# Optimization experiments

Measured on AMD Instinct MI355X. Metric: run time of the kernel, lower is better.

Reference implementation:

```python
import jax, jax.numpy as jnp
import numpy as np

B = 1024
INPUT_DIM = 768
NUM_CLASSES = 5
NUM_PRIMARY_CAPS = 32
PRIMARY_CAP_DIM = 8
ROUTING_CAP_DIM = 16
NUM_ITER = 3
PROJ_DIM = 256 * 6 * 6  # 9216
NUM_IN_CAPS = NUM_PRIMARY_CAPS * 16  # conv output is 4x4 spatial -> 512


def squash(t, axis=-1):
    sq = jnp.sum(t * t, axis=axis, keepdims=True)
    scale = sq / (1.0 + sq)
    return scale * t / jnp.sqrt(sq + 1e-8)


def setup_inputs() -> dict:
    key = jax.random.key(0)
    k = jax.random.split(key, 6)
    x = jax.random.normal(k[0], (B, INPUT_DIM), dtype=jnp.float32)
    W1 = jax.random.normal(k[1], (INPUT_DIM, PROJ_DIM), dtype=jnp.float32) * 0.02
    b1 = jnp.zeros((PROJ_DIM,), dtype=jnp.float32)
    convW = jax.random.normal(k[2], (NUM_PRIMARY_CAPS * PRIMARY_CAP_DIM, 256, 3, 3), dtype=jnp.float32) * 0.02  # OIHW
    convB = jnp.zeros((NUM_PRIMARY_CAPS * PRIMARY_CAP_DIM,), dtype=jnp.float32)
    # matches torch.randn init in RoutingCapsules: [num_in, num_out, out_dim, in_dim]
    Wr = jax.random.normal(k[3], (NUM_IN_CAPS, NUM_CLASSES, ROUTING_CAP_DIM, PRIMARY_CAP_DIM), dtype=jnp.float32)
    return {"x": x, "W1": W1, "b1": b1, "convW": convW, "convB": convB, "Wr": Wr}


def reference(x, W1, b1, convW, convB, Wr):
    # feature projection (dropout is identity in eval)
    h = jax.nn.relu(x @ W1 + b1)
    h = h.reshape(-1, 256, 6, 6)
    # primary capsules conv: k=3, s=1, pad=0 -> [B, 256, 4, 4]
    out = jax.lax.conv_general_dilated(h, convW, window_strides=(1, 1), padding='VALID',
                                       dimension_numbers=('NCHW', 'OIHW', 'NCHW'))
    out = out + convB[None, :, None, None]
    bsz = out.shape[0]
    out = out.reshape(bsz, NUM_PRIMARY_CAPS, PRIMARY_CAP_DIM, -1)      # [B,32,8,16]
    out = jnp.transpose(out, (0, 1, 3, 2)).reshape(bsz, -1, PRIMARY_CAP_DIM)  # [B,512,8]
    u = squash(out, axis=-1)
    # prediction vectors u_hat: [B, in_caps, out_caps, out_dim]
    u_hat = jnp.einsum('nodi,bni->bnod', Wr, u)
    # dynamic routing
    b_logits = jnp.zeros((bsz, NUM_IN_CAPS, NUM_CLASSES, 1), dtype=u_hat.dtype)
    v = None
    for it in range(NUM_ITER):
        c = jax.nn.softmax(b_logits, axis=2)
        s = jnp.sum(c * u_hat, axis=1)  # [B, out_caps, out_dim]
        v = squash(s, axis=-1)
        if it < NUM_ITER - 1:
            agreement = jnp.sum(u_hat * v[:, None], axis=-1, keepdims=True)
            b_logits = b_logits + agreement
    class_probs = jnp.sqrt(jnp.sum(v * v, axis=-1))
    return (class_probs, v)
```

## Files before the change

### kernel.cpp

```cpp
#include <hip/hip_runtime.h>
#include <hip/hip_fp16.h>

#define BSZ   1024
#define INDIM 768
#define PROJ  9216
#define NCAP  512
#define NCLS  5
#define K2    2304

typedef __bf16    bf16x8 __attribute__((ext_vector_type(8)));
typedef _Float16  f16x8  __attribute__((ext_vector_type(8)));
typedef float     f32x4  __attribute__((ext_vector_type(4)));
typedef _Float16  h2     __attribute__((ext_vector_type(2)));

static __device__ __forceinline__ unsigned short f2bf(float f) {
  unsigned int x = __float_as_uint(f);
  return (unsigned short)((x + 0x7fffu + ((x >> 16) & 1u)) >> 16);
}
static __device__ __forceinline__ unsigned short f2h(float f) {
  return __builtin_bit_cast(unsigned short, (_Float16)f);
}

#if defined(__has_builtin)
#if __has_builtin(__builtin_amdgcn_fdot2)
#define HAVE_FDOT2 1
#endif
#endif
static __device__ __forceinline__ float fdot2(h2 a, h2 b, float c) {
#ifdef HAVE_FDOT2
  return __builtin_amdgcn_fdot2(a, b, c, false);
#else
  return c + (float)a[0] * (float)b[0] + (float)a[1] * (float)b[1];
#endif
}
static __device__ __forceinline__ h2 u2h2(unsigned int u) {
  return __builtin_bit_cast(h2, u);
}

static __device__ __forceinline__ void gload16(const void* g, void* l) {
  auto gp = reinterpret_cast<const unsigned int __attribute__((address_space(1)))*>(
      (unsigned long long)g);
  auto lp = reinterpret_cast<unsigned int __attribute__((address_space(3)))*>(
      (unsigned long long)l);
  __builtin_amdgcn_global_load_lds(gp, lp, 16, 0, 0);
}

__global__ __launch_bounds__(256) void mfma_gemm_bk64(
    const unsigned short* __restrict__ A,
    const unsigned short* __restrict__ Bt,
    const float* __restrict__ bias,
    unsigned short* __restrict__ Cout,
    int M, int N, int K) {
  __shared__ __align__(16) unsigned short smem[32768];
  const int t    = threadIdx.x;
  const int bn   = blockIdx.x * 128;
  const int bm   = blockIdx.y * 128;
  const int lane = t & 63, wid = t >> 6;
  const int wm   = (wid >> 1) * 64;
  const int wn   = (wid & 1) * 64;
  const int l15  = lane & 15, kb = lane >> 4;

  const unsigned short* asrc[4];
  const unsigned short* bsrc[4];
#pragma unroll
  for (int cc = 0; cc < 4; ++cc) {
    const int c = t + cc * 256;
    const int row = c >> 3, seg = c & 7;
    const int sk = (seg ^ (row & 7)) << 3;
    asrc[cc] = A  + (size_t)(bm + row) * K + sk;
    bsrc[cc] = Bt + (size_t)(bn + row) * K + sk;
  }

  int aoff[4][2], boff[4][2];
#pragma unroll
  for (int i = 0; i < 4; ++i)
#pragma unroll
    for (int kk = 0; kk < 2; ++kk) {
      const int ra = wm + i * 16 + l15, sa = kk * 4 + kb;
      aoff[i][kk] = ra * 64 + ((sa ^ (ra & 7)) << 3);
      const int rb = wn + i * 16 + l15;
      boff[i][kk] = 8192 + rb * 64 + ((sa ^ (rb & 7)) << 3);
    }

  f32x4 acc[4][4];
#pragma unroll
  for (int i = 0; i < 4; ++i)
#pragma unroll
    for (int j = 0; j < 4; ++j)
#pragma unroll
      for (int q = 0; q < 4; ++q) acc[i][j][q] = 0.f;

  const int nk = K >> 6;
  auto stage = [&](int ks, int buf) {
    const int ko = ks << 6;
    unsigned short* sb = &smem[buf * 16384];
#pragma unroll
    for (int cc = 0; cc < 4; ++cc) {
      gload16(asrc[cc] + ko, sb + (t + cc * 256) * 8);
      gload16(bsrc[cc] + ko, sb + 8192 + (t + cc * 256) * 8);
    }
  };

  stage(0, 0);
  __syncthreads();

  int buf = 0;
  for (int ks = 0; ks < nk; ++ks) {
    if (ks + 1 < nk) stage(ks + 1, buf ^ 1);
    const unsigned short* base = &smem[buf * 16384];
    bf16x8 af[4][2], bfr[4][2];
#pragma unroll
    for (int i = 0; i < 4; ++i)
#pragma unroll
      for (int kk = 0; kk < 2; ++kk) {
        af[i][kk]  = *(const bf16x8*)(base + aoff[i][kk]);
        bfr[i][kk] = *(const bf16x8*)(base + boff[i][kk]);
      }
#pragma unroll
    for (int kk = 0; kk < 2; ++kk)
#pragma unroll
      for (int i = 0; i < 4; ++i)
#pragma unroll
        for (int j = 0; j < 4; ++j)
          acc[i][j] = __builtin_amdgcn_mfma_f32_16x16x32_bf16(af[i][kk], bfr[j][kk], acc[i][j], 0, 0, 0);
    __syncthreads();
    buf ^= 1;
  }

#pragma unroll
  for (int j = 0; j < 4; ++j) {
    const int col = bn + wn + j * 16 + l15;
    const float bv = bias[col];
#pragma unroll
    for (int i = 0; i < 4; ++i)
#pragma unroll
      for (int q = 0; q < 4; ++q) {
        const int row = bm + wm + i * 16 + kb * 4 + q;
        Cout[(size_t)row * N + col] = f2bf(fmaxf(acc[i][j][q] + bv, 0.f));
      }
  }
}

__global__ __launch_bounds__(256) void conv_gemm_sq(
    const unsigned short* __restrict__ ht,
    const unsigned short* __restrict__ Wt2,
    const float* __restrict__ convB,
    unsigned short* __restrict__ U) {
  __shared__ __align__(16) unsigned short smem[24576];
  const int t    = threadIdx.x;
  const int bn   = blockIdx.x * 128;
  const int bm   = blockIdx.y * 64;
  const int lane = t & 63, wid = t >> 6;
  const int l15  = lane & 15, kb = lane >> 4;

  const unsigned short* asrc[2];
#pragma unroll
  for (int cc = 0; cc < 2; ++cc) {
    const int c = t + cc * 256;
    const int row = c >> 3, seg = c & 7;
    const int gr = bm + row, b = gr >> 4, p = gr & 15;
    const int spb = (p >> 2) * 6 + (p & 3);
    asrc[cc] = ht + (size_t)b * PROJ + spb * 256 + ((seg ^ (row & 7)) << 3);
  }
  const unsigned short* bsrc[4];
#pragma unroll
  for (int cc = 0; cc < 4; ++cc) {
    const int c = t + cc * 256;
    const int row = c >> 3, seg = c & 7;
    bsrc[cc] = Wt2 + (size_t)(bn + row) * K2 + ((seg ^ (row & 7)) << 3);
  }

  int aoff[4][2], boff[2][2];
#pragma unroll
  for (int i = 0; i < 4; ++i)
#pragma unroll
    for (int kk = 0; kk < 2; ++kk) {
      const int row = i * 16 + l15, seg = kk * 4 + kb;
      aoff[i][kk] = row * 64 + ((seg ^ (row & 7)) << 3);
    }
#pragma unroll
  for (int j = 0; j < 2; ++j)
#pragma unroll
    for (int kk = 0; kk < 2; ++kk) {
      const int row = wid * 32 + j * 16 + l15, seg = kk * 4 + kb;
      boff[j][kk] = 4096 + row * 64 + ((seg ^ (row & 7)) << 3);
    }

  f32x4 acc[4][2];
#pragma unroll
  for (int i = 0; i < 4; ++i)
#pragma unroll
    for (int j = 0; j < 2; ++j)
#pragma unroll
      for (int q = 0; q < 4; ++q) acc[i][j][q] = 0.f;

  auto stage = [&](int ks, int buf) {
    const int tap  = ks >> 2;
    const int aofs = (tap + 3 * (tap / 3)) * 256 + ((ks & 3) << 6);
    const int bofs = ks << 6;
    unsigned short* sb = &smem[buf * 12288];
    gload16(asrc[0] + aofs, sb + t * 8);
    gload16(asrc[1] + aofs, sb + t * 8 + 2048);
    gload16(bsrc[0] + bofs, sb + 4096 + t * 8);
    gload16(bsrc[1] + bofs, sb + 4096 + t * 8 + 2048);
    gload16(bsrc[2] + bofs, sb + 4096 + t * 8 + 4096);
    gload16(bsrc[3] + bofs, sb + 4096 + t * 8 + 6144);
  };

  stage(0, 0);
  __syncthreads();

  int buf = 0;
  for (int ks = 0; ks < 36; ++ks) {
    if (ks + 1 < 36) stage(ks + 1, buf ^ 1);
    const unsigned short* base = &smem[buf * 12288];
    bf16x8 af[4][2], bfr[2][2];
#pragma unroll
    for (int i = 0; i < 4; ++i)
#pragma unroll
      for (int kk = 0; kk < 2; ++kk) af[i][kk] = *(const bf16x8*)(base + aoff[i][kk]);
#pragma unroll
    for (int j = 0; j < 2; ++j)
#pragma unroll
      for (int kk = 0; kk < 2; ++kk) bfr[j][kk] = *(const bf16x8*)(base + boff[j][kk]);
#pragma unroll
    for (int kk = 0; kk < 2; ++kk)
#pragma unroll
      for (int i = 0; i < 4; ++i)
#pragma unroll
        for (int j = 0; j < 2; ++j)
          acc[i][j] = __builtin_amdgcn_mfma_f32_16x16x32_bf16(af[i][kk], bfr[j][kk], acc[i][j], 0, 0, 0);
    __syncthreads();
    buf ^= 1;
  }

#pragma unroll
  for (int j = 0; j < 2; ++j) {
    const int oc  = bn + wid * 32 + j * 16 + l15;
    const int cap = oc >> 3, ii = oc & 7;
    const float bv = convB[oc];
#pragma unroll
    for (int i = 0; i < 4; ++i) {
#pragma unroll
      for (int q = 0; q < 4; ++q) {
        const int row = bm + i * 16 + kb * 4 + q;
        const int b = row >> 4, p = row & 15;
        const float val = acc[i][j][q] + bv;
        float sq = val * val;
        sq += __shfl_xor(sq, 1);
        sq += __shfl_xor(sq, 2);
        sq += __shfl_xor(sq, 4);
        const float scale = sq / (1.f + sq) / sqrtf(sq + 1e-8f);
        U[(size_t)b * 4096 + cap * 128 + p * 8 + ii] = f2h(val * scale);
      }
    }
  }
}

#define TP_BLOCKS (288 * 24)
#define NX_ITEMS (BSZ * INDIM / 4)
#define NW_ITEMS (NCAP * 640 / 4)
#define NWT_ITEMS (NCAP * 80)
#define NC_ITEMS 65536
#define NB_ITEMS PROJ
#define EW_TOTAL (NX_ITEMS + NW_ITEMS + NWT_ITEMS + NC_ITEMS + NB_ITEMS)
#define EW_BLOCKS (EW_TOTAL / 256)

__global__ __launch_bounds__(256) void prep_all(
    const float* __restrict__ W1, unsigned short* __restrict__ w1t,
    const float* __restrict__ x, unsigned short* __restrict__ xb,
    const float* __restrict__ Wr, __half2* __restrict__ wrh,
    unsigned short* __restrict__ wrh_t,
    const float* __restrict__ convW, unsigned short* __restrict__ wt2,
    const float* __restrict__ b1, float* __restrict__ pb1) {
  __shared__ float tile[32][33];
  if (blockIdx.x < TP_BLOCKS) {
    const int tb = blockIdx.x;
    const int n0 = (tb % 288) * 32, k0 = (tb / 288) * 32;
    const int r = threadIdx.x >> 3, c = (threadIdx.x & 7) * 4;
    float4 v = *(const float4*)(W1 + (size_t)(k0 + r) * PROJ + n0 + c);
    tile[r][c] = v.x; tile[r][c + 1] = v.y; tile[r][c + 2] = v.z; tile[r][c + 3] = v.w;
    __syncthreads();
    ushort4 o;
    o.x = f2bf(tile[c + 0][r]); o.y = f2bf(tile[c + 1][r]);
    o.z = f2bf(tile[c + 2][r]); o.w = f2bf(tile[c + 3][r]);
    const int nn = n0 + r;
    const int prow = (nn % 36) * 256 + nn / 36;
    *(ushort4*)(w1t + (size_t)prow * INDIM + k0 + c) = o;
    return;
  }
  const int id = (blockIdx.x - TP_BLOCKS) * 256 + threadIdx.x;
  if (id < NX_ITEMS) {
    float4 v = ((const float4*)x)[id];
    ushort4 o;
    o.x = f2bf(v.x); o.y = f2bf(v.y); o.z = f2bf(v.z); o.w = f2bf(v.w);
    ((ushort4*)xb)[id] = o;
  } else if (id < NX_ITEMS + NW_ITEMS) {
    const int i = id - NX_ITEMS;
    float4 v = ((const float4*)Wr)[i];
    wrh[i * 2]     = __floats2half2_rn(v.x, v.y);
    wrh[i * 2 + 1] = __floats2half2_rn(v.z, v.w);
  } else if (id < NX_ITEMS + NW_ITEMS + NWT_ITEMS) {
    const int i = id - NX_ITEMS - NW_ITEMS;
    const int od = i / NCAP, n = i % NCAP;
    const float4 a = *(const float4*)(Wr + (size_t)n * 640 + od * 8);
    const float4 b = *(const float4*)(Wr + (size_t)n * 640 + od * 8 + 4);
    __half2 h0 = __floats2half2_rn(a.x, a.y), h1 = __floats2half2_rn(a.z, a.w);
    __half2 h2v = __floats2half2_rn(b.x, b.y), h3 = __floats2half2_rn(b.z, b.w);
    uint4 st = make_uint4(__builtin_bit_cast(unsigned int, h0),
                          __builtin_bit_cast(unsigned int, h1),
                          __builtin_bit_cast(unsigned int, h2v),
                          __builtin_bit_cast(unsigned int, h3));
    *(uint4*)(wrh_t + (size_t)od * 4096 + n * 8) = st;
  } else if (id < NX_ITEMS + NW_ITEMS + NWT_ITEMS + NC_ITEMS) {
    const int i = id - NX_ITEMS - NW_ITEMS - NWT_ITEMS;
    const int oc = i >> 8, ic = i & 255;
    const float* s = convW + (size_t)i * 9;
#pragma unroll
    for (int tap = 0; tap < 9; ++tap)
      wt2[(size_t)oc * K2 + tap * 256 + ic] = f2bf(s[tap]);
  } else if (id < EW_TOTAL) {
    const int n = id - NX_ITEMS - NW_ITEMS - NWT_ITEMS - NC_ITEMS;
    pb1[(n % 36) * 256 + n / 36] = b1[n];
  }
}

__global__ __launch_bounds__(256) void s0v0_gemm(
    const unsigned short* __restrict__ U,
    const unsigned short* __restrict__ WrhT,
    float* __restrict__ v0) {
  __shared__ float red[4][16][16];
  __shared__ float sl[16][17];
  __shared__ float scl[16];
  const int bt = blockIdx.x, o = blockIdx.y;
  const int t = threadIdx.x, wid = t >> 6, lane = t & 63;
  const int l15 = lane & 15, kb = lane >> 4;
  const int gb = bt * 16;

  f32x4 acc;
  acc[0] = 0.f; acc[1] = 0.f; acc[2] = 0.f; acc[3] = 0.f;
  const unsigned short* abase = WrhT + (size_t)(o * 16 + l15) * 4096 + kb * 8;
  const unsigned short* bbase = U + (size_t)(gb + l15) * 4096 + kb * 8;
  const int k0b = wid * 1024;
#pragma unroll 4
  for (int k0 = k0b; k0 < k0b + 1024; k0 += 32) {
    const f16x8 av = __builtin_bit_cast(f16x8, *(const uint4*)(abase + k0));
    const f16x8 bv = __builtin_bit_cast(f16x8, *(const uint4*)(bbase + k0));
    acc = __builtin_amdgcn_mfma_f32_16x16x32_f16(av, bv, acc, 0, 0, 0);
  }
#pragma unroll
  for (int q = 0; q < 4; ++q) red[wid][kb * 4 + q][l15] = acc[q];
  __syncthreads();
  const int row = t >> 4, col = t & 15;
  const float s = 0.2f * (red[0][row][col] + red[1][row][col] +
                          red[2][row][col] + red[3][row][col]);
  sl[row][col] = s;
  __syncthreads();
  if (t < 16) {
    float sq = 0.f;
#pragma unroll
    for (int r = 0; r < 16; ++r) { const float xx = sl[r][t]; sq += xx * xx; }
    scl[t] = sq / (1.f + sq) / sqrtf(sq + 1e-8f);
  }
  __syncthreads();
  v0[(size_t)(gb + col) * 80 + o * 16 + row] = s * scl[col];
}

__global__ __launch_bounds__(512) void uhat_p1(
    const unsigned short* __restrict__ U,
    const unsigned short* __restrict__ Wrh,
    const float* __restrict__ v0,
    unsigned short* __restrict__ uhat,
    float* __restrict__ sp1,
    int b0, int CB) {
  __shared__ float sred[8][16][80];
  const int mt = blockIdx.x, q = blockIdx.y;
  const int t = threadIdx.x, wid = t >> 6, lane = t & 63;
  const int l15 = lane & 15, kb = lane >> 4;
  const int bm = mt * 16;
  const int gb = b0 + bm;

  f32x4 vreg[5];
#pragma unroll
  for (int jn = 0; jn < 5; ++jn)
    vreg[jn] = *(const f32x4*)(v0 + (size_t)(gb + l15) * 80 + jn * 16 + kb * 4);

  f32x4 sacc[5];
#pragma unroll
  for (int jn = 0; jn < 5; ++jn)
#pragma unroll
    for (int qq = 0; qq < 4; ++qq) sacc[jn][qq] = 0.f;

  const uint4 zz = make_uint4(0, 0, 0, 0);
#pragma unroll
  for (int i = 0; i < 8; ++i) {
    const int n = q * 64 + wid * 8 + i;
    uint4 av = zz;
    if (kb == 0) av = *(const uint4*)(U + (size_t)(gb + l15) * 4096 + n * 8);
    const f16x8 uf = __builtin_bit_cast(f16x8, av);
    f32x4 cfr[5];
#pragma unroll
    for (int jn = 0; jn < 5; ++jn) {
      uint4 wv = zz;
      if (kb == 0) wv = *(const uint4*)(Wrh + (size_t)n * 640 + (jn * 16 + l15) * 8);
      f32x4 z;
      z[0] = 0.f; z[1] = 0.f; z[2] = 0.f; z[3] = 0.f;
      cfr[jn] = __builtin_amdgcn_mfma_f32_16x16x32_f16(
          __builtin_bit_cast(f16x8, wv), uf, z, 0, 0, 0);
      ushort4 st;
      st.x = f2h(cfr[jn][0]); st.y = f2h(cfr[jn][1]);
      st.z = f2h(cfr[jn][2]); st.w = f2h(cfr[jn][3]);
      *(ushort4*)(uhat + ((size_t)(bm + l15) * 512 + n) * 80 + jn * 16 + kb * 4) = st;
    }
    float a[5];
#pragma unroll
    for (int jn = 0; jn < 5; ++jn) {
      float d = cfr[jn][0] * vreg[jn][0] + cfr[jn][1] * vreg[jn][1] +
                cfr[jn][2] * vreg[jn][2] + cfr[jn][3] * vreg[jn][3];
      d += __shfl_xor(d, 16);
      d += __shfl_xor(d, 32);
      a[jn] = d;
    }
    float m = fmaxf(fmaxf(fmaxf(a[0], a[1]), fmaxf(a[2], a[3])), a[4]);
    float c[5], es = 0.f;
#pragma unroll
    for (int o = 0; o < 5; ++o) { c[o] = __expf(a[o] - m); es += c[o]; }
    const float inv = 1.f / es;
#pragma unroll
    for (int jn = 0; jn < 5; ++jn) {
      const float cc = c[jn] * inv;
#pragma unroll
      for (int qq = 0; qq < 4; ++qq) sacc[jn][qq] += cc * cfr[jn][qq];
    }
  }

#pragma unroll
  for (int jn = 0; jn < 5; ++jn)
#pragma unroll
    for (int qq = 0; qq < 4; ++qq)
      sred[wid][l15][jn * 16 + kb * 4 + qq] = sacc[jn][qq];
  __syncthreads();
#pragma unroll
  for (int k = 0; k < 3; ++k) {
    const int id = t + k * 512;
    if (id < 1280) {
      const int bb = id / 80, od = id % 80;
      float val = 0.f;
#pragma unroll
      for (int w = 0; w < 8; ++w) val += sred[w][bb][od];
      sp1[((size_t)q * BSZ + gb + bb) * 80 + od] = val;
    }
  }
}

__global__ __launch_bounds__(128) void v01_k(
    const float* __restrict__ sp1, const float* __restrict__ v0,
    float* __restrict__ v01, int b0) {
  const int b = b0 + blockIdx.x, t = threadIdx.x;
  if (t < 80) {
    float s = 0.f;
#pragma unroll
    for (int g = 0; g < 8; ++g) s += sp1[((size_t)g * BSZ + b) * 80 + t];
    float sq = s * s;
    sq += __shfl_xor(sq, 1);
    sq += __shfl_xor(sq, 2);
    sq += __shfl_xor(sq, 4);
    sq += __shfl_xor(sq, 8);
    const float scale = sq / (1.f + sq) / sqrtf(sq + 1e-8f);
    v01[(size_t)b * 80 + t] = v0[(size_t)b * 80 + t] + s * scale;
  }
}

__global__ __launch_bounds__(256) void route_pass2(
    const unsigned short* __restrict__ uhat,
    const float* __restrict__ vsum_in,
    float* __restrict__ out, int b0) {
  __shared__ unsigned int vph2[40];
  __shared__ float red[4][2][40];
  const int bl = blockIdx.x;
  const int b  = b0 + bl;
  const int t  = threadIdx.x;

  float v0r = 0.f;
  if (t < 80) {
    v0r = vsum_in[(size_t)b * 80 + t];
    const float vnext = __shfl_down(v0r, 1);
    if ((t & 1) == 0)
      vph2[t >> 1] = __builtin_bit_cast(unsigned int, __floats2half2_rn(v0r, vnext));
  }
  __syncthreads();

  const int p = t >> 1, h = t & 1;
  float acc[5][8];
#pragma unroll
  for (int o = 0; o < 5; ++o)
#pragma unroll
    for (int j = 0; j < 8; ++j) acc[o][j] = 0.f;

  const unsigned short* ub = uhat + (size_t)bl * 40960;
  for (int c4 = 0; c4 < 4; ++c4) {
    const int n = c4 * 128 + p;
    const unsigned short* row = ub + n * 80 + h * 8;
    uint4 uv[5];
#pragma unroll
    for (int o = 0; o < 5; ++o) uv[o] = *(const uint4*)(row + o * 16);
    float ap[5];
#pragma unroll
    for (int o = 0; o < 5; ++o) {
      const int vb = o * 8 + h * 4;
      float a = fdot2(u2h2(uv[o].x), u2h2(vph2[vb]), 0.f);
      a = fdot2(u2h2(uv[o].y), u2h2(vph2[vb + 1]), a);
      a = fdot2(u2h2(uv[o].z), u2h2(vph2[vb + 2]), a);
      a = fdot2(u2h2(uv[o].w), u2h2(vph2[vb + 3]), a);
      ap[o] = a + __shfl_xor(a, 1);
    }
    float m = ap[0];
#pragma unroll
    for (int o = 1; o < 5; ++o) m = fmaxf(m, ap[o]);
    float es = 0.f, e[5];
#pragma unroll
    for (int o = 0; o < 5; ++o) { e[o] = __expf(ap[o] - m); es += e[o]; }
    const float inv = 1.f / es;
#pragma unroll
    for (int o = 0; o < 5; ++o) {
      const float cc = e[o] * inv;
      h2 hx = u2h2(uv[o].x), hy = u2h2(uv[o].y), hz = u2h2(uv[o].z), hw = u2h2(uv[o].w);
      acc[o][0] += cc * (float)hx[0]; acc[o][1] += cc * (float)hx[1];
      acc[o][2] += cc * (float)hy[0]; acc[o][3] += cc * (float)hy[1];
      acc[o][4] += cc * (float)hz[0]; acc[o][5] += cc * (float)hz[1];
      acc[o][6] += cc * (float)hw[0]; acc[o][7] += cc * (float)hw[1];
    }
  }

#pragma unroll
  for (int off = 2; off <= 32; off <<= 1)
#pragma unroll
    for (int o = 0; o < 5; ++o)
#pragma unroll
      for (int j = 0; j < 8; ++j) acc[o][j] += __shfl_xor(acc[o][j], off);
  const int wid = t >> 6, lane = t & 63;
  if (lane < 2) {
#pragma unroll
    for (int o = 0; o < 5; ++o)
#pragma unroll
      for (int j = 0; j < 8; ++j) red[wid][lane][o * 8 + j] = acc[o][j];
  }
  __syncthreads();

  if (t < 80) {
    const int o = t >> 4, d = t & 15, hh = d >> 3, dl = d & 7;
    const int c = o * 8 + dl;
    float s = red[0][hh][c] + red[1][hh][c] + red[2][hh][c] + red[3][hh][c];
    float sq = s * s;
    sq += __shfl_xor(sq, 1);
    sq += __shfl_xor(sq, 2);
    sq += __shfl_xor(sq, 4);
    sq += __shfl_xor(sq, 8);
    const float scale = sq / (1.f + sq) / sqrtf(sq + 1e-8f);
    const float vn = s * scale;
    out[5 * BSZ + (size_t)b * 80 + t] = vn;
    float vv = vn * vn;
    vv += __shfl_xor(vv, 1);
    vv += __shfl_xor(vv, 2);
    vv += __shfl_xor(vv, 4);
    vv += __shfl_xor(vv, 8);
    if ((t & 15) == 0) out[(size_t)b * 5 + o] = sqrtf(vv);
  }
}

extern "C" void kernel_launch(void* const* d_in, const int* in_sizes, int n_in,
                              void* d_out, int out_size, void* d_ws, size_t ws_size,
                              hipStream_t stream) {
  const float* x     = (const float*)d_in[0];
  const float* W1    = (const float*)d_in[1];
  const float* b1    = (const float*)d_in[2];
  const float* convW = (const float*)d_in[3];
  const float* convB = (const float*)d_in[4];
  const float* Wr    = (const float*)d_in[5];
  float* out = (float*)d_out;

  char* base = (char*)d_ws;
  size_t off = 0;
  auto alloc = [&](size_t bytes) { size_t o = off; off = (off + bytes + 255) & ~(size_t)255; return o; };
  const size_t o_wrh  = alloc((size_t)NCAP * 640 * 2);
  const size_t o_wrt  = alloc((size_t)80 * 4096 * 2);
  const size_t o_u    = alloc((size_t)BSZ * 4096 * 2);
  const size_t o_sp1  = alloc((size_t)8 * BSZ * 80 * 4);
  const size_t o_v0   = alloc((size_t)BSZ * 80 * 4);
  const size_t o_v01  = alloc((size_t)BSZ * 80 * 4);
  const size_t o_pool = off;
  size_t poff = o_pool;
  auto palloc = [&](size_t bytes) { size_t o = poff; poff = (poff + bytes + 255) & ~(size_t)255; return o; };
  const size_t o_ht  = palloc((size_t)BSZ * PROJ * 2);
  const size_t o_w1t = palloc((size_t)PROJ * INDIM * 2);
  const size_t o_xb  = palloc((size_t)BSZ * INDIM * 2);
  const size_t o_wt2 = palloc((size_t)256 * K2 * 2);
  const size_t o_pb1 = palloc((size_t)PROJ * 4);

  unsigned short* ht   = (unsigned short*)(base + o_ht);
  unsigned short* w1t  = (unsigned short*)(base + o_w1t);
  unsigned short* xb   = (unsigned short*)(base + o_xb);
  unsigned short* wt2  = (unsigned short*)(base + o_wt2);
  float*          pb1  = (float*)(base + o_pb1);
  unsigned short* wrh  = (unsigned short*)(base + o_wrh);
  unsigned short* wrt  = (unsigned short*)(base + o_wrt);
  unsigned short* u    = (unsigned short*)(base + o_u);
  float*          sp1  = (float*)(base + o_sp1);
  float*          v0   = (float*)(base + o_v0);
  float*          v01  = (float*)(base + o_v01);
  unsigned short* uhat = (unsigned short*)(base + o_pool);

  prep_all<<<TP_BLOCKS + EW_BLOCKS, 256, 0, stream>>>(
      W1, w1t, x, xb, Wr, (__half2*)wrh, wrt, convW, wt2, b1, pb1);

  mfma_gemm_bk64<<<dim3(PROJ / 128, BSZ / 128), 256, 0, stream>>>(
      xb, w1t, pb1, ht, BSZ, PROJ, INDIM);

  conv_gemm_sq<<<dim3(2, 256), 256, 0, stream>>>(ht, wt2, convB, u);

  s0v0_gemm<<<dim3(BSZ / 16, 5), 256, 0, stream>>>(u, wrt, v0);

  const size_t pool_sz = ws_size > o_pool ? ws_size - o_pool : 0;
  int CB = 1024;
  while (CB > 16 && (size_t)CB * 512 * 80 * 2 > pool_sz) CB >>= 1;
  for (int b0 = 0; b0 < BSZ; b0 += CB) {
    uhat_p1<<<dim3(CB / 16, 8), 512, 0, stream>>>(u, wrh, v0, uhat, sp1, b0, CB);
    v01_k<<<CB, 128, 0, stream>>>(sp1, v0, v01, b0);
    route_pass2<<<CB, 256, 0, stream>>>(uhat, v01, out, b0);
  }
}
```

Measured before the change: 152.4 us.

## Shrink conv GEMM tile to 64x64 and regroup uhat layout per 16-sample tile

The primary-capsule conv GEMM tile shrinks from 64x128 to 64x64 with a 2x2 warp grid, doubling the block count from 512 to 1024 and cutting shared memory per block. This is meant to improve occupancy and load balance across CUs, at the cost of less operand reuse per block. Separately, the uhat buffer is re-laid out as [tile][capsule][16 samples][80] so the MFMA store in uhat_p1 writes contiguous rows. route_pass2 indexing is updated to match, giving it a 1280-element stride between capsules.

```diff
diff --git a/kernel.cpp b/kernel.cpp
--- a/kernel.cpp
+++ b/kernel.cpp
@@ -141,19 +141,21 @@
   }
 }
 
-__global__ __launch_bounds__(256) void conv_gemm_sq(
+__global__ __launch_bounds__(256) void conv_gemm_sq64(
     const unsigned short* __restrict__ ht,
     const unsigned short* __restrict__ Wt2,
     const float* __restrict__ convB,
     unsigned short* __restrict__ U) {
-  __shared__ __align__(16) unsigned short smem[24576];
+  __shared__ __align__(16) unsigned short smem[16384];
   const int t    = threadIdx.x;
-  const int bn   = blockIdx.x * 128;
+  const int bn   = blockIdx.x * 64;
   const int bm   = blockIdx.y * 64;
   const int lane = t & 63, wid = t >> 6;
+  const int wm   = (wid >> 1) * 32, wn = (wid & 1) * 32;
   const int l15  = lane & 15, kb = lane >> 4;
 
   const unsigned short* asrc[2];
+  const unsigned short* bsrc[2];
 #pragma unroll
   for (int cc = 0; cc < 2; ++cc) {
     const int c = t + cc * 256;
@@ -161,34 +163,23 @@
     const int gr = bm + row, b = gr >> 4, p = gr & 15;
     const int spb = (p >> 2) * 6 + (p & 3);
     asrc[cc] = ht + (size_t)b * PROJ + spb * 256 + ((seg ^ (row & 7)) << 3);
-  }
-  const unsigned short* bsrc[4];
-#pragma unroll
-  for (int cc = 0; cc < 4; ++cc) {
-    const int c = t + cc * 256;
-    const int row = c >> 3, seg = c & 7;
     bsrc[cc] = Wt2 + (size_t)(bn + row) * K2 + ((seg ^ (row & 7)) << 3);
   }
 
-  int aoff[4][2], boff[2][2];
-#pragma unroll
-  for (int i = 0; i < 4; ++i)
+  int aoff[2][2], boff[2][2];
+#pragma unroll
+  for (int i = 0; i < 2; ++i)
 #pragma unroll
     for (int kk = 0; kk < 2; ++kk) {
-      const int row = i * 16 + l15, seg = kk * 4 + kb;
-      aoff[i][kk] = row * 64 + ((seg ^ (row & 7)) << 3);
-    }
-#pragma unroll
-  for (int j = 0; j < 2; ++j)
-#pragma unroll
-    for (int kk = 0; kk < 2; ++kk) {
-      const int row = wid * 32 + j * 16 + l15, seg = kk * 4 + kb;
-      boff[j][kk] = 4096 + row * 64 + ((seg ^ (row & 7)) << 3);
-    }
-
-  f32x4 acc[4][2];
-#pragma unroll
-  for (int i = 0; i < 4; ++i)
+      const int ra = wm + i * 16 + l15, sa = kk * 4 + kb;
+      aoff[i][kk] = ra * 64 + ((sa ^ (ra & 7)) << 3);
+      const int rb = wn + i * 16 + l15;
+      boff[i][kk] = 4096 + rb * 64 + ((sa ^ (rb & 7)) << 3);
+    }
+
+  f32x4 acc[2][2];
+#pragma unroll
+  for (int i = 0; i < 2; ++i)
 #pragma unroll
     for (int j = 0; j < 2; ++j)
 #pragma unroll
@@ -198,13 +189,11 @@
     const int tap  = ks >> 2;
     const int aofs = (tap + 3 * (tap / 3)) * 256 + ((ks & 3) << 6);
     const int bofs = ks << 6;
-    unsigned short* sb = &smem[buf * 12288];
+    unsigned short* sb = &smem[buf * 8192];
     gload16(asrc[0] + aofs, sb + t * 8);
-    gload16(asrc[1] + aofs, sb + t * 8 + 2048);
+    gload16(asrc[1] + aofs, sb + (t + 256) * 8);
     gload16(bsrc[0] + bofs, sb + 4096 + t * 8);
-    gload16(bsrc[1] + bofs, sb + 4096 + t * 8 + 2048);
-    gload16(bsrc[2] + bofs, sb + 4096 + t * 8 + 4096);
-    gload16(bsrc[3] + bofs, sb + 4096 + t * 8 + 6144);
+    gload16(bsrc[1] + bofs, sb + 4096 + (t + 256) * 8);
   };
 
   stage(0, 0);
@@ -213,20 +202,19 @@
   int buf = 0;
   for (int ks = 0; ks < 36; ++ks) {
     if (ks + 1 < 36) stage(ks + 1, buf ^ 1);
-    const unsigned short* base = &smem[buf * 12288];
-    bf16x8 af[4][2], bfr[2][2];
-#pragma unroll
-    for (int i = 0; i < 4; ++i)
-#pragma unroll
-      for (int kk = 0; kk < 2; ++kk) af[i][kk] = *(const bf16x8*)(base + aoff[i][kk]);
-#pragma unroll
-    for (int j = 0; j < 2; ++j)
-#pragma unroll
-      for (int kk = 0; kk < 2; ++kk) bfr[j][kk] = *(const bf16x8*)(base + boff[j][kk]);
+    const unsigned short* base = &smem[buf * 8192];
+    bf16x8 af[2][2], bfr[2][2];
+#pragma unroll
+    for (int i = 0; i < 2; ++i)
+#pragma unroll
+      for (int kk = 0; kk < 2; ++kk) {
+        af[i][kk]  = *(const bf16x8*)(base + aoff[i][kk]);
+        bfr[i][kk] = *(const bf16x8*)(base + boff[i][kk]);
+      }
 #pragma unroll
     for (int kk = 0; kk < 2; ++kk)
 #pragma unroll
-      for (int i = 0; i < 4; ++i)
+      for (int i = 0; i < 2; ++i)
 #pragma unroll
         for (int j = 0; j < 2; ++j)
           acc[i][j] = __builtin_amdgcn_mfma_f32_16x16x32_bf16(af[i][kk], bfr[j][kk], acc[i][j], 0, 0, 0);
@@ -236,14 +224,14 @@
 
 #pragma unroll
   for (int j = 0; j < 2; ++j) {
-    const int oc  = bn + wid * 32 + j * 16 + l15;
+    const int oc  = bn + wn + j * 16 + l15;
     const int cap = oc >> 3, ii = oc & 7;
     const float bv = convB[oc];
 #pragma unroll
-    for (int i = 0; i < 4; ++i) {
+    for (int i = 0; i < 2; ++i) {
 #pragma unroll
       for (int q = 0; q < 4; ++q) {
-        const int row = bm + i * 16 + kb * 4 + q;
+        const int row = bm + wm + i * 16 + kb * 4 + q;
         const int b = row >> 4, p = row & 15;
         const float val = acc[i][j][q] + bv;
         float sq = val * val;
@@ -377,8 +365,7 @@
   const int mt = blockIdx.x, q = blockIdx.y;
   const int t = threadIdx.x, wid = t >> 6, lane = t & 63;
   const int l15 = lane & 15, kb = lane >> 4;
-  const int bm = mt * 16;
-  const int gb = b0 + bm;
+  const int gb = b0 + mt * 16;
 
   f32x4 vreg[5];
 #pragma unroll
@@ -390,6 +377,8 @@
   for (int jn = 0; jn < 5; ++jn)
 #pragma unroll
     for (int qq = 0; qq < 4; ++qq) sacc[jn][qq] = 0.f;
+
+  unsigned short* ubase = uhat + (size_t)mt * 512 * 1280;
 
   const uint4 zz = make_uint4(0, 0, 0, 0);
 #pragma unroll
@@ -410,7 +399,7 @@
       ushort4 st;
       st.x = f2h(cfr[jn][0]); st.y = f2h(cfr[jn][1]);
       st.z = f2h(cfr[jn][2]); st.w = f2h(cfr[jn][3]);
-      *(ushort4*)(uhat + ((size_t)(bm + l15) * 512 + n) * 80 + jn * 16 + kb * 4) = st;
+      *(ushort4*)(ubase + ((size_t)n * 16 + l15) * 80 + jn * 16 + kb * 4) = st;
     }
     float a[5];
 #pragma unroll
@@ -497,10 +486,10 @@
 #pragma unroll
     for (int j = 0; j < 8; ++j) acc[o][j] = 0.f;
 
-  const unsigned short* ub = uhat + (size_t)bl * 40960;
+  const unsigned short* ub = uhat + ((size_t)(bl >> 4) * 512 * 16 + (bl & 15)) * 80;
   for (int c4 = 0; c4 < 4; ++c4) {
     const int n = c4 * 128 + p;
-    const unsigned short* row = ub + n * 80 + h * 8;
+    const unsigned short* row = ub + (size_t)n * 1280 + h * 8;
     uint4 uv[5];
 #pragma unroll
     for (int o = 0; o < 5; ++o) uv[o] = *(const uint4*)(row + o * 16);
@@ -616,7 +605,7 @@
   mfma_gemm_bk64<<<dim3(PROJ / 128, BSZ / 128), 256, 0, stream>>>(
       xb, w1t, pb1, ht, BSZ, PROJ, INDIM);
 
-  conv_gemm_sq<<<dim3(2, 256), 256, 0, stream>>>(ht, wt2, convB, u);
+  conv_gemm_sq64<<<dim3(4, 256), 256, 0, stream>>>(ht, wt2, convB, u);
 
   s0v0_gemm<<<dim3(BSZ / 16, 5), 256, 0, stream>>>(u, wrt, v0);
 
```

New measurement: 163.8 us. +7.5%, slower.
